# Performance work log

Measured on AMD Instinct MI355X. Metric: run time of the kernel, lower is better.

The kernel has to match this reference:

```python
import jax, jax.numpy as jnp
import numpy as np

B, C, Q, D = 64, 1024, 256, 128
NEG = -1e30  # VERY_NEGATIVE_NUMBER


def setup_inputs() -> dict:
    key = jax.random.key(0)
    k1, k2, k3, k4, k5, k6 = jax.random.split(key, 6)
    return {
        "x_cont": jax.random.normal(k1, (B, C, D), dtype=jnp.float32),
        "x_ques": jax.random.normal(k2, (B, Q, D), dtype=jnp.float32),
        "c_mask": jnp.ones((B, C), dtype=jnp.float32),
        "q_mask": jnp.ones((B, Q), dtype=jnp.float32),
        "W0": jax.random.uniform(k3, (D, 1), jnp.float32, -0.1, 0.1),
        "W1": jax.random.uniform(k4, (D, 1), jnp.float32, -0.1, 0.1),
        "W2": jax.random.uniform(k5, (1, 1, D), jnp.float32, -0.1, 0.1),
        "bias": jnp.zeros((1,), dtype=jnp.float32),
    }


def reference(x_cont, x_ques, c_mask, q_mask, W0, W1, W2, bias):
    # Trilinear similarity S[b,c,q] = x_cont.W0 + x_ques.W1 + (x_cont*W2).x_ques^T + bias
    s0 = x_cont @ W0                                   # [B,C,1]
    s1 = jnp.swapaxes(x_ques @ W1, 1, 2)               # [B,1,Q]
    s2 = jnp.einsum('bcd,bqd->bcq', x_cont * W2, x_ques)  # [B,C,Q]
    S = s0 + s1 + s2 + bias                            # [B,C,Q]

    qm = q_mask[:, None, :]                            # [B,1,Q]
    cm = c_mask[:, :, None]                            # [B,C,1]
    S_ = jax.nn.softmax(S + NEG * (1.0 - qm), axis=-1)           # row softmax [B,C,Q]
    S_T = jnp.swapaxes(jax.nn.softmax(S + NEG * (1.0 - cm), axis=1), 1, 2)  # [B,Q,C]

    c2q = S_ @ x_ques                                  # [B,C,D]
    q2c = (S_ @ S_T) @ x_cont                          # [B,C,D]
    return jnp.concatenate([x_cont, c2q, x_cont * c2q, x_cont * q2c], axis=-1)
```

## Files before the change

### kernel.cpp

```cpp
#include <hip/hip_runtime.h>
#include <math.h>

#define BB 64
#define CC 1024
#define QQ 256
#define DD 128
#define NEGV (-1.0e30f)

typedef short bf8 __attribute__((ext_vector_type(8)));
typedef short bf4 __attribute__((ext_vector_type(4)));
typedef float f4v __attribute__((ext_vector_type(4)));

__device__ __forceinline__ short f2bf(float f) {
    unsigned u = __builtin_bit_cast(unsigned, f);
    u += 0x7FFFu + ((u >> 16) & 1u);
    return (short)(u >> 16);
}
__device__ __forceinline__ float bf2f(short s) {
    unsigned u = ((unsigned)(unsigned short)s) << 16;
    return __builtin_bit_cast(float, u);
}

__global__ __launch_bounds__(256, 2) void k0_all(
        const float* __restrict__ xc, const float* __restrict__ xq,
        const float* __restrict__ W0, const float* __restrict__ W1,
        const float* __restrict__ W2,
        const float* __restrict__ c_mask, const float* __restrict__ q_mask,
        float* __restrict__ s0m, float* __restrict__ s1m,
        short* __restrict__ xc_bf, short* __restrict__ xqw_bf,
        short* __restrict__ xcT_bf, short* __restrict__ xqT_bf) {
    __shared__ float tile[64][129];
    int bid = blockIdx.x;
    const float *src, *W, *mask;
    float* sm; short *rm, *tr;
    int b, tl, R; bool use2;
    if (bid < 1024) {
        b = ((bid >> 7) << 3) | (bid & 7); tl = (bid >> 3) & 15; R = CC;
        src = xc; W = W0; mask = c_mask; sm = s0m; rm = xc_bf; tr = xcT_bf; use2 = false;
    } else {
        int q = bid - 1024;
        b = ((q >> 5) << 3) | (q & 7); tl = (q >> 3) & 3; R = QQ;
        src = xq; W = W1; mask = q_mask; sm = s1m; rm = xqw_bf; tr = xqT_bf; use2 = true;
    }
    int r0 = tl * 64;
    int t = threadIdx.x;
    int c4 = t & 31, rr = t >> 5;
    float4 wv = ((const float4*)W)[c4];
    float4 sc4 = use2 ? ((const float4*)W2)[c4] : make_float4(1.f, 1.f, 1.f, 1.f);
    const float* sb = src + ((size_t)b * R + r0) * DD;
    #pragma unroll
    for (int p = 0; p < 8; ++p) {
        int row = rr + p * 8;
        float4 g = *(const float4*)&sb[(size_t)row * DD + c4 * 4];
        bf4 o;
        o[0] = f2bf(g.x * sc4.x); o[1] = f2bf(g.y * sc4.y);
        o[2] = f2bf(g.z * sc4.z); o[3] = f2bf(g.w * sc4.w);
        *(bf4*)&rm[((size_t)(b * R + r0 + row)) * DD + c4 * 4] = o;
        float part = g.x * wv.x + g.y * wv.y + g.z * wv.z + g.w * wv.w;
        #pragma unroll
        for (int off = 1; off < 32; off <<= 1) part += __shfl_xor(part, off, 64);
        if ((t & 31) == 0)
            sm[(size_t)b * R + r0 + row] =
                part + NEGV * (1.0f - mask[(size_t)b * R + r0 + row]);
        tile[row][c4 * 4 + 0] = g.x; tile[row][c4 * 4 + 1] = g.y;
        tile[row][c4 * 4 + 2] = g.z; tile[row][c4 * 4 + 3] = g.w;
    }
    __syncthreads();
    int rj = (t & 7) * 8;
    #pragma unroll
    for (int pp = 0; pp < 4; ++pp) {
        int d = pp * 32 + (t >> 3);
        bf8 o;
        #pragma unroll
        for (int j = 0; j < 8; ++j) o[j] = f2bf(tile[rj + j][d]);
        *(bf8*)&tr[((size_t)(b * DD + d)) * R + r0 + rj] = o;
    }
}

#define SCP 1032
#define S2P 264

__global__ __launch_bounds__(256, 3) void k1_colsm(
        const short* __restrict__ xc_bf, const short* __restrict__ xcT_bf,
        const short* __restrict__ xqw_bf, const float* __restrict__ s0m,
        short* __restrict__ AT) {
    __shared__ __align__(16) short sc[16][SCP];
    __shared__ float invl[16];

    int bid = blockIdx.x;
    int qt = (bid >> 3) & 15;
    int b = ((bid >> 7) << 3) | (bid & 7);
    int q0 = qt * 16;
    int t = threadIdx.x, w = t >> 6, l = t & 63;
    int quad = l >> 4, l16 = l & 15;

    bf8 bq[4];
    {
        const short* qp = &xqw_bf[(size_t)(b * QQ + q0 + l16) * DD + quad * 8];
        #pragma unroll
        for (int ks = 0; ks < 4; ++ks) bq[ks] = *(const bf8*)&qp[ks * 32];
    }

    const short* abase = &xc_bf[(size_t)(b * CC + w * 16 + l16) * DD + quad * 8];
    const float* s0base = &s0m[b * CC + w * 16 + quad * 4];
    bf8 cur[4];
    #pragma unroll
    for (int ks = 0; ks < 4; ++ks) cur[ks] = *(const bf8*)&abase[ks * 32];
    #pragma unroll
    for (int ct = 0; ct < 16; ++ct) {
        bf8 nxt[4];
        if (ct < 15) {
            const short* ar = abase + (size_t)(ct + 1) * 64 * DD;
            #pragma unroll
            for (int ks = 0; ks < 4; ++ks) nxt[ks] = *(const bf8*)&ar[ks * 32];
        }
        f4v acc = {0.f, 0.f, 0.f, 0.f};
        #pragma unroll
        for (int ks = 0; ks < 4; ++ks)
            acc = __builtin_amdgcn_mfma_f32_16x16x32_bf16(cur[ks], bq[ks], acc, 0, 0, 0);
        f4v s0v = *(const f4v*)&s0base[ct * 64];
        bf4 ov;
        #pragma unroll
        for (int r = 0; r < 4; ++r) ov[r] = f2bf(acc[r] + s0v[r]);
        *(bf4*)&sc[l16][ct * 64 + w * 16 + quad * 4] = ov;
        if (ct < 15) {
            #pragma unroll
            for (int ks = 0; ks < 4; ++ks) cur[ks] = nxt[ks];
        }
    }
    __syncthreads();

    const short* b0base = &xcT_bf[(size_t)(b * DD + w * 32 + l16) * CC + quad * 8];
    const short* b1base = b0base + (size_t)16 * CC;
    bf8 pb[3][4];
    #pragma unroll
    for (int i = 0; i < 3; ++i) {
        #pragma unroll
        for (int ks = 0; ks < 2; ++ks) {
            pb[i][ks]     = *(const bf8*)&b0base[i * 64 + ks * 32];
            pb[i][2 + ks] = *(const bf8*)&b1base[i * 64 + ks * 32];
        }
    }

    {
        int q = t >> 4, k = t & 15;
        float m = -3.0e38f;
        #pragma unroll 8
        for (int i = 0; i < 64; ++i) m = fmaxf(m, bf2f(sc[q][k + 16 * i]));
        #pragma unroll
        for (int off = 1; off < 16; off <<= 1) m = fmaxf(m, __shfl_xor(m, off, 64));
        float sum = 0.f;
        #pragma unroll 8
        for (int i = 0; i < 64; ++i) {
            int idx = k + 16 * i;
            float e = __expf(bf2f(sc[q][idx]) - m);
            sc[q][idx] = f2bf(e);
            sum += e;
        }
        #pragma unroll
        for (int off = 1; off < 16; off <<= 1) sum += __shfl_xor(sum, off, 64);
        if (k == 0) invl[q] = 1.0f / sum;
    }
    __syncthreads();

    f4v acc0 = {0.f, 0.f, 0.f, 0.f}, acc1 = {0.f, 0.f, 0.f, 0.f};
    #pragma unroll
    for (int ct = 0; ct < 16; ++ct) {
        bf8 c00 = pb[0][0], c01 = pb[0][1], c10 = pb[0][2], c11 = pb[0][3];
        #pragma unroll
        for (int i = 0; i < 2; ++i)
            #pragma unroll
            for (int j = 0; j < 4; ++j) pb[i][j] = pb[i + 1][j];
        if (ct + 3 < 16) {
            #pragma unroll
            for (int ks = 0; ks < 2; ++ks) {
                pb[2][ks]     = *(const bf8*)&b0base[(ct + 3) * 64 + ks * 32];
                pb[2][2 + ks] = *(const bf8*)&b1base[(ct + 3) * 64 + ks * 32];
            }
        }
        bf8 a0 = *(const bf8*)&sc[l16][ct * 64 + quad * 8];
        bf8 a1 = *(const bf8*)&sc[l16][ct * 64 + 32 + quad * 8];
        acc0 = __builtin_amdgcn_mfma_f32_16x16x32_bf16(a0, c00, acc0, 0, 0, 0);
        acc0 = __builtin_amdgcn_mfma_f32_16x16x32_bf16(a1, c01, acc0, 0, 0, 0);
        acc1 = __builtin_amdgcn_mfma_f32_16x16x32_bf16(a0, c10, acc1, 0, 0, 0);
        acc1 = __builtin_amdgcn_mfma_f32_16x16x32_bf16(a1, c11, acc1, 0, 0, 0);
    }
    {
        bf4 o0, o1;
        #pragma unroll
        for (int r = 0; r < 4; ++r) {
            float il = invl[quad * 4 + r];
            o0[r] = f2bf(acc0[r] * il);
            o1[r] = f2bf(acc1[r] * il);
        }
        int d0 = w * 32 + l16;
        *(bf4*)&AT[(size_t)(b * DD + d0) * QQ + q0 + quad * 4] = o0;
        *(bf4*)&AT[(size_t)(b * DD + d0 + 16) * QQ + q0 + quad * 4] = o1;
    }
}

__global__ __launch_bounds__(256, 3) void k2_rowsm(
        const float* __restrict__ xc, const short* __restrict__ xc_bf,
        const short* __restrict__ xqw_bf, const short* __restrict__ xqT_bf,
        const short* __restrict__ AT, const float* __restrict__ s1m,
        float* __restrict__ out) {
    __shared__ __align__(16) short sc2[32][S2P];
    __shared__ float invl2[32];

    int bid = blockIdx.x;
    int cb = (bid >> 3) & 31;
    int b = ((bid >> 8) << 3) | (bid & 7);
    int c0g = cb * 32;
    int t = threadIdx.x, w = t >> 6, l = t & 63;
    int quad = l >> 4, l16 = l & 15;

    bf8 bc0[4], bc1[4];
    {
        const short* p0 = &xc_bf[(size_t)(b * CC + c0g + l16) * DD + quad * 8];
        const short* p1 = p0 + 16 * DD;
        #pragma unroll
        for (int ks = 0; ks < 4; ++ks) {
            bc0[ks] = *(const bf8*)&p0[ks * 32];
            bc1[ks] = *(const bf8*)&p1[ks * 32];
        }
    }

    const short* abase = &xqw_bf[(size_t)(b * QQ + w * 16 + l16) * DD + quad * 8];
    const float* s1base = &s1m[b * QQ + w * 16 + quad * 4];
    bf8 cur[4];
    #pragma unroll
    for (int ks = 0; ks < 4; ++ks) cur[ks] = *(const bf8*)&abase[ks * 32];
    #pragma unroll
    for (int qt = 0; qt < 4; ++qt) {
        bf8 nxt[4];
        if (qt < 3) {
            const short* ar = abase + (size_t)(qt + 1) * 64 * DD;
            #pragma unroll
            for (int ks = 0; ks < 4; ++ks) nxt[ks] = *(const bf8*)&ar[ks * 32];
        }
        f4v acc0 = {0.f, 0.f, 0.f, 0.f}, acc1 = {0.f, 0.f, 0.f, 0.f};
        #pragma unroll
        for (int ks = 0; ks < 4; ++ks) {
            acc0 = __builtin_amdgcn_mfma_f32_16x16x32_bf16(cur[ks], bc0[ks], acc0, 0, 0, 0);
            acc1 = __builtin_amdgcn_mfma_f32_16x16x32_bf16(cur[ks], bc1[ks], acc1, 0, 0, 0);
        }
        int qbase = qt * 64 + w * 16 + quad * 4;
        f4v sv = *(const f4v*)&s1base[qt * 64];
        bf4 o0, o1;
        #pragma unroll
        for (int r = 0; r < 4; ++r) {
            o0[r] = f2bf(acc0[r] + sv[r]);
            o1[r] = f2bf(acc1[r] + sv[r]);
        }
        *(bf4*)&sc2[l16][qbase] = o0;
        *(bf4*)&sc2[16 + l16][qbase] = o1;
        if (qt < 3) {
            #pragma unroll
            for (int ks = 0; ks < 4; ++ks) cur[ks] = nxt[ks];
        }
    }
    __syncthreads();

    const short* gq = &xqT_bf[(size_t)(b * DD + w * 32 + l16) * QQ + quad * 8];
    const short* ga = &AT[(size_t)(b * DD + w * 32 + l16) * QQ + quad * 8];
    bf8 pb[3][4];
    #pragma unroll
    for (int i = 0; i < 3; ++i) {
        #pragma unroll
        for (int ks = 0; ks < 2; ++ks) {
            pb[i][ks]     = *(const bf8*)&gq[i * 64 + ks * 32];
            pb[i][2 + ks] = *(const bf8*)&gq[(size_t)16 * QQ + i * 64 + ks * 32];
        }
    }

    {
        int c = t >> 3, k = t & 7;
        float m = -3.0e38f;
        #pragma unroll 8
        for (int i = 0; i < 32; ++i) m = fmaxf(m, bf2f(sc2[c][k + 8 * i]));
        #pragma unroll
        for (int off = 1; off < 8; off <<= 1) m = fmaxf(m, __shfl_xor(m, off, 64));
        float sum = 0.f;
        #pragma unroll 8
        for (int i = 0; i < 32; ++i) {
            int idx = k + 8 * i;
            float e = __expf(bf2f(sc2[c][idx]) - m);
            sc2[c][idx] = f2bf(e);
            sum += e;
        }
        #pragma unroll
        for (int off = 1; off < 8; off <<= 1) sum += __shfl_xor(sum, off, 64);
        if (k == 0) invl2[c] = 1.0f / sum;
    }
    __syncthreads();

    f4v ac[2][2], aq[2][2];
    f4v zz = {0.f, 0.f, 0.f, 0.f};
    #pragma unroll
    for (int i = 0; i < 2; ++i)
        #pragma unroll
        for (int j = 0; j < 2; ++j) { ac[i][j] = zz; aq[i][j] = zz; }
    #pragma unroll
    for (int tl = 0; tl < 8; ++tl) {
        bf8 c00 = pb[0][0], c01 = pb[0][1], c10 = pb[0][2], c11 = pb[0][3];
        #pragma unroll
        for (int i = 0; i < 2; ++i)
            #pragma unroll
            for (int j = 0; j < 4; ++j) pb[i][j] = pb[i + 1][j];
        if (tl + 3 < 8) {
            int nt = tl + 3;
            const short* gs = (nt < 4) ? (gq + (size_t)(nt) * 64)
                                       : (ga + (size_t)(nt - 4) * 64);
            #pragma unroll
            for (int ks = 0; ks < 2; ++ks) {
                pb[2][ks]     = *(const bf8*)&gs[ks * 32];
                pb[2][2 + ks] = *(const bf8*)&gs[(size_t)16 * QQ + ks * 32];
            }
        }
        int qoff = (tl & 3) * 64;
        bf8 a00 = *(const bf8*)&sc2[l16][qoff + quad * 8];
        bf8 a01 = *(const bf8*)&sc2[l16][qoff + 32 + quad * 8];
        bf8 a10 = *(const bf8*)&sc2[16 + l16][qoff + quad * 8];
        bf8 a11 = *(const bf8*)&sc2[16 + l16][qoff + 32 + quad * 8];
        if (tl < 4) {
            ac[0][0] = __builtin_amdgcn_mfma_f32_16x16x32_bf16(a00, c00, ac[0][0], 0, 0, 0);
            ac[0][0] = __builtin_amdgcn_mfma_f32_16x16x32_bf16(a01, c01, ac[0][0], 0, 0, 0);
            ac[0][1] = __builtin_amdgcn_mfma_f32_16x16x32_bf16(a00, c10, ac[0][1], 0, 0, 0);
            ac[0][1] = __builtin_amdgcn_mfma_f32_16x16x32_bf16(a01, c11, ac[0][1], 0, 0, 0);
            ac[1][0] = __builtin_amdgcn_mfma_f32_16x16x32_bf16(a10, c00, ac[1][0], 0, 0, 0);
            ac[1][0] = __builtin_amdgcn_mfma_f32_16x16x32_bf16(a11, c01, ac[1][0], 0, 0, 0);
            ac[1][1] = __builtin_amdgcn_mfma_f32_16x16x32_bf16(a10, c10, ac[1][1], 0, 0, 0);
            ac[1][1] = __builtin_amdgcn_mfma_f32_16x16x32_bf16(a11, c11, ac[1][1], 0, 0, 0);
        } else {
            aq[0][0] = __builtin_amdgcn_mfma_f32_16x16x32_bf16(a00, c00, aq[0][0], 0, 0, 0);
            aq[0][0] = __builtin_amdgcn_mfma_f32_16x16x32_bf16(a01, c01, aq[0][0], 0, 0, 0);
            aq[0][1] = __builtin_amdgcn_mfma_f32_16x16x32_bf16(a00, c10, aq[0][1], 0, 0, 0);
            aq[0][1] = __builtin_amdgcn_mfma_f32_16x16x32_bf16(a01, c11, aq[0][1], 0, 0, 0);
            aq[1][0] = __builtin_amdgcn_mfma_f32_16x16x32_bf16(a10, c00, aq[1][0], 0, 0, 0);
            aq[1][0] = __builtin_amdgcn_mfma_f32_16x16x32_bf16(a11, c01, aq[1][0], 0, 0, 0);
            aq[1][1] = __builtin_amdgcn_mfma_f32_16x16x32_bf16(a10, c10, aq[1][1], 0, 0, 0);
            aq[1][1] = __builtin_amdgcn_mfma_f32_16x16x32_bf16(a11, c11, aq[1][1], 0, 0, 0);
        }
    }

    #pragma unroll
    for (int cf = 0; cf < 2; ++cf)
        #pragma unroll
        for (int r = 0; r < 4; ++r) {
            int cl = cf * 16 + quad * 4 + r;
            int c = c0g + cl;
            float il = invl2[cl];
            const float* xrow = xc + (size_t)(b * CC + c) * DD;
            float* orow = out + (size_t)(b * CC + c) * (4 * DD);
            #pragma unroll
            for (int df = 0; df < 2; ++df) {
                int d = w * 32 + df * 16 + l16;
                float xv = xrow[d];
                float c2v = ac[cf][df][r] * il;
                float q2v = aq[cf][df][r] * il;
                orow[d] = xv;
                orow[DD + d] = c2v;
                orow[2 * DD + d] = xv * c2v;
                orow[3 * DD + d] = xv * q2v;
            }
        }
}

extern "C" void kernel_launch(void* const* d_in, const int* in_sizes, int n_in,
                              void* d_out, int out_size, void* d_ws, size_t ws_size,
                              hipStream_t stream) {
    const float* x_cont = (const float*)d_in[0];
    const float* x_ques = (const float*)d_in[1];
    const float* c_mask = (const float*)d_in[2];
    const float* q_mask = (const float*)d_in[3];
    const float* W0     = (const float*)d_in[4];
    const float* W1     = (const float*)d_in[5];
    const float* W2     = (const float*)d_in[6];
    float* out = (float*)d_out;

    char* ws = (char*)d_ws;
    float* s0m    = (float*)ws;  ws += (size_t)BB * CC * 4;
    float* s1m    = (float*)ws;  ws += (size_t)BB * QQ * 4;
    short* xc_bf  = (short*)ws;  ws += (size_t)BB * CC * DD * 2;
    short* xqw_bf = (short*)ws;  ws += (size_t)BB * QQ * DD * 2;
    short* xcT_bf = (short*)ws;  ws += (size_t)BB * CC * DD * 2;
    short* xqT_bf = (short*)ws;  ws += (size_t)BB * QQ * DD * 2;
    short* AT     = (short*)ws;

    k0_all<<<BB * 16 + BB * 4, 256, 0, stream>>>(x_cont, x_ques, W0, W1, W2,
                                                 c_mask, q_mask, s0m, s1m,
                                                 xc_bf, xqw_bf, xcT_bf, xqT_bf);
    k1_colsm<<<BB * 16, 256, 0, stream>>>(xc_bf, xcT_bf, xqw_bf, s0m, AT);
    k2_rowsm<<<BB * 32, 256, 0, stream>>>(x_cont, xc_bf, xqw_bf, xqT_bf, AT, s1m, out);
}
```

Before: 296.4 us.

## Stage transposed B operands through LDS with coalesced loads in both kernels

Both the column-softmax and row-softmax kernels now load the transposed xc/xq/AT operand tiles with coalesced per-thread 16-byte reads into an LDS staging buffer, then read MFMA fragments from LDS. This replaces the per-lane strided global fragment loads and the register ring buffer. The first GEMM is deepened to four tiles of prefetch, the softmax passes use vectorized bf8 LDS reads and writes, and k2's launch bounds are raised to 4 blocks. The cost is four __syncthreads per pair of tiles and extra LDS usage, which may limit occupancy.

```diff
diff --git a/kernel.cpp b/kernel.cpp
--- a/kernel.cpp
+++ b/kernel.cpp
@@ -79,12 +79,64 @@
 
 #define SCP 1032
 #define S2P 264
+#define XTP 72
+
+#define K1_LDA(G, S, CT)                                                 \
+    {                                                                    \
+        const short* ar_ = abase + (size_t)(CT) * 64 * DD;               \
+        G[0] = *(const bf8*)&ar_[0];  G[1] = *(const bf8*)&ar_[32];      \
+        G[2] = *(const bf8*)&ar_[64]; G[3] = *(const bf8*)&ar_[96];      \
+        S = *(const f4v*)&s0base[(CT) * 64];                             \
+    }
+
+#define K1_STEPA(G, S, CT)                                                            \
+    {                                                                                 \
+        f4v acc = {0.f, 0.f, 0.f, 0.f};                                               \
+        acc = __builtin_amdgcn_mfma_f32_16x16x32_bf16(G[0], bq[0], acc, 0, 0, 0);     \
+        acc = __builtin_amdgcn_mfma_f32_16x16x32_bf16(G[1], bq[1], acc, 0, 0, 0);     \
+        acc = __builtin_amdgcn_mfma_f32_16x16x32_bf16(G[2], bq[2], acc, 0, 0, 0);     \
+        acc = __builtin_amdgcn_mfma_f32_16x16x32_bf16(G[3], bq[3], acc, 0, 0, 0);     \
+        bf4 ov;                                                                       \
+        ov[0] = f2bf(acc[0] + S[0]); ov[1] = f2bf(acc[1] + S[1]);                     \
+        ov[2] = f2bf(acc[2] + S[2]); ov[3] = f2bf(acc[3] + S[3]);                     \
+        *(bf4*)&sc[l16][(CT) * 64 + w * 16 + quad * 4] = ov;                          \
+        if ((CT) + 4 < 16) K1_LDA(G, S, (CT) + 4);                                    \
+    }
+
+#define K1_STG(GS, NXT)                                                  \
+    {                                                                    \
+        *(bf8*)&xct[dr][c8 * 8] = GS[0];                                 \
+        *(bf8*)&xct[dr + 32][c8 * 8] = GS[1];                            \
+        *(bf8*)&xct[dr + 64][c8 * 8] = GS[2];                            \
+        *(bf8*)&xct[dr + 96][c8 * 8] = GS[3];                            \
+        if ((NXT) < 16) {                                                \
+            GS[0] = *(const bf8*)&tbase[(NXT) * 64];                     \
+            GS[1] = *(const bf8*)&tbase[(size_t)32 * CC + (NXT) * 64];   \
+            GS[2] = *(const bf8*)&tbase[(size_t)64 * CC + (NXT) * 64];   \
+            GS[3] = *(const bf8*)&tbase[(size_t)96 * CC + (NXT) * 64];   \
+        }                                                                \
+    }
+
+#define K1_CSTEP(CT)                                                               \
+    {                                                                              \
+        bf8 a0 = *(const bf8*)&sc[l16][(CT) * 64 + quad * 8];                      \
+        bf8 b0 = *(const bf8*)&xct[w * 32 + l16][quad * 8];                        \
+        acc0 = __builtin_amdgcn_mfma_f32_16x16x32_bf16(a0, b0, acc0, 0, 0, 0);     \
+        bf8 b1 = *(const bf8*)&xct[w * 32 + 16 + l16][quad * 8];                   \
+        acc1 = __builtin_amdgcn_mfma_f32_16x16x32_bf16(a0, b1, acc1, 0, 0, 0);     \
+        bf8 a1 = *(const bf8*)&sc[l16][(CT) * 64 + 32 + quad * 8];                 \
+        bf8 b2 = *(const bf8*)&xct[w * 32 + l16][32 + quad * 8];                   \
+        acc0 = __builtin_amdgcn_mfma_f32_16x16x32_bf16(a1, b2, acc0, 0, 0, 0);     \
+        bf8 b3 = *(const bf8*)&xct[w * 32 + 16 + l16][32 + quad * 8];              \
+        acc1 = __builtin_amdgcn_mfma_f32_16x16x32_bf16(a1, b3, acc1, 0, 0, 0);     \
+    }
 
 __global__ __launch_bounds__(256, 3) void k1_colsm(
         const short* __restrict__ xc_bf, const short* __restrict__ xcT_bf,
         const short* __restrict__ xqw_bf, const float* __restrict__ s0m,
         short* __restrict__ AT) {
     __shared__ __align__(16) short sc[16][SCP];
+    __shared__ __align__(16) short xct[DD][XTP];
     __shared__ float invl[16];
 
     int bid = blockIdx.x;
@@ -103,59 +155,54 @@
 
     const short* abase = &xc_bf[(size_t)(b * CC + w * 16 + l16) * DD + quad * 8];
     const float* s0base = &s0m[b * CC + w * 16 + quad * 4];
-    bf8 cur[4];
-    #pragma unroll
-    for (int ks = 0; ks < 4; ++ks) cur[ks] = *(const bf8*)&abase[ks * 32];
-    #pragma unroll
-    for (int ct = 0; ct < 16; ++ct) {
-        bf8 nxt[4];
-        if (ct < 15) {
-            const short* ar = abase + (size_t)(ct + 1) * 64 * DD;
-            #pragma unroll
-            for (int ks = 0; ks < 4; ++ks) nxt[ks] = *(const bf8*)&ar[ks * 32];
-        }
-        f4v acc = {0.f, 0.f, 0.f, 0.f};
-        #pragma unroll
-        for (int ks = 0; ks < 4; ++ks)
-            acc = __builtin_amdgcn_mfma_f32_16x16x32_bf16(cur[ks], bq[ks], acc, 0, 0, 0);
-        f4v s0v = *(const f4v*)&s0base[ct * 64];
-        bf4 ov;
-        #pragma unroll
-        for (int r = 0; r < 4; ++r) ov[r] = f2bf(acc[r] + s0v[r]);
-        *(bf4*)&sc[l16][ct * 64 + w * 16 + quad * 4] = ov;
-        if (ct < 15) {
-            #pragma unroll
-            for (int ks = 0; ks < 4; ++ks) cur[ks] = nxt[ks];
-        }
-    }
+    bf8 gA[4], gB[4], gC[4], gD[4];
+    f4v sA, sB, sC, sD;
+    K1_LDA(gA, sA, 0); K1_LDA(gB, sB, 1); K1_LDA(gC, sC, 2); K1_LDA(gD, sD, 3);
+    #pragma unroll
+    for (int c4t = 0; c4t < 16; c4t += 4) {
+        K1_STEPA(gA, sA, c4t + 0);
+        K1_STEPA(gB, sB, c4t + 1);
+        K1_STEPA(gC, sC, c4t + 2);
+        K1_STEPA(gD, sD, c4t + 3);
+    }
+
+    int c8 = t & 7, dr = t >> 3;
+    const short* tbase = &xcT_bf[(size_t)(b * DD + dr) * CC + c8 * 8];
+    bf8 gS0[4], gS1[4];
+    gS0[0] = *(const bf8*)&tbase[0];
+    gS0[1] = *(const bf8*)&tbase[(size_t)32 * CC];
+    gS0[2] = *(const bf8*)&tbase[(size_t)64 * CC];
+    gS0[3] = *(const bf8*)&tbase[(size_t)96 * CC];
+    gS1[0] = *(const bf8*)&tbase[64];
+    gS1[1] = *(const bf8*)&tbase[(size_t)32 * CC + 64];
+    gS1[2] = *(const bf8*)&tbase[(size_t)64 * CC + 64];
+    gS1[3] = *(const bf8*)&tbase[(size_t)96 * CC + 64];
+
     __syncthreads();
-
-    const short* b0base = &xcT_bf[(size_t)(b * DD + w * 32 + l16) * CC + quad * 8];
-    const short* b1base = b0base + (size_t)16 * CC;
-    bf8 pb[3][4];
-    #pragma unroll
-    for (int i = 0; i < 3; ++i) {
-        #pragma unroll
-        for (int ks = 0; ks < 2; ++ks) {
-            pb[i][ks]     = *(const bf8*)&b0base[i * 64 + ks * 32];
-            pb[i][2 + ks] = *(const bf8*)&b1base[i * 64 + ks * 32];
-        }
-    }
 
     {
         int q = t >> 4, k = t & 15;
+        bf8 v[8];
+        #pragma unroll
+        for (int j = 0; j < 8; ++j) v[j] = *(const bf8*)&sc[q][k * 8 + j * 128];
         float m = -3.0e38f;
-        #pragma unroll 8
-        for (int i = 0; i < 64; ++i) m = fmaxf(m, bf2f(sc[q][k + 16 * i]));
+        #pragma unroll
+        for (int j = 0; j < 8; ++j)
+            #pragma unroll
+            for (int e = 0; e < 8; ++e) m = fmaxf(m, bf2f(v[j][e]));
         #pragma unroll
         for (int off = 1; off < 16; off <<= 1) m = fmaxf(m, __shfl_xor(m, off, 64));
         float sum = 0.f;
-        #pragma unroll 8
-        for (int i = 0; i < 64; ++i) {
-            int idx = k + 16 * i;
-            float e = __expf(bf2f(sc[q][idx]) - m);
-            sc[q][idx] = f2bf(e);
-            sum += e;
+        #pragma unroll
+        for (int j = 0; j < 8; ++j) {
+            bf8 o;
+            #pragma unroll
+            for (int e = 0; e < 8; ++e) {
+                float ex = __expf(bf2f(v[j][e]) - m);
+                sum += ex;
+                o[e] = f2bf(ex);
+            }
+            *(bf8*)&sc[q][k * 8 + j * 128] = o;
         }
         #pragma unroll
         for (int off = 1; off < 16; off <<= 1) sum += __shfl_xor(sum, off, 64);
@@ -165,25 +212,15 @@
 
     f4v acc0 = {0.f, 0.f, 0.f, 0.f}, acc1 = {0.f, 0.f, 0.f, 0.f};
     #pragma unroll
-    for (int ct = 0; ct < 16; ++ct) {
-        bf8 c00 = pb[0][0], c01 = pb[0][1], c10 = pb[0][2], c11 = pb[0][3];
-        #pragma unroll
-        for (int i = 0; i < 2; ++i)
-            #pragma unroll
-            for (int j = 0; j < 4; ++j) pb[i][j] = pb[i + 1][j];
-        if (ct + 3 < 16) {
-            #pragma unroll
-            for (int ks = 0; ks < 2; ++ks) {
-                pb[2][ks]     = *(const bf8*)&b0base[(ct + 3) * 64 + ks * 32];
-                pb[2][2 + ks] = *(const bf8*)&b1base[(ct + 3) * 64 + ks * 32];
-            }
-        }
-        bf8 a0 = *(const bf8*)&sc[l16][ct * 64 + quad * 8];
-        bf8 a1 = *(const bf8*)&sc[l16][ct * 64 + 32 + quad * 8];
-        acc0 = __builtin_amdgcn_mfma_f32_16x16x32_bf16(a0, c00, acc0, 0, 0, 0);
-        acc0 = __builtin_amdgcn_mfma_f32_16x16x32_bf16(a1, c01, acc0, 0, 0, 0);
-        acc1 = __builtin_amdgcn_mfma_f32_16x16x32_bf16(a0, c10, acc1, 0, 0, 0);
-        acc1 = __builtin_amdgcn_mfma_f32_16x16x32_bf16(a1, c11, acc1, 0, 0, 0);
+    for (int ct = 0; ct < 16; ct += 2) {
+        K1_STG(gS0, ct + 2);
+        __syncthreads();
+        K1_CSTEP(ct);
+        __syncthreads();
+        K1_STG(gS1, ct + 3);
+        __syncthreads();
+        K1_CSTEP(ct + 1);
+        __syncthreads();
     }
     {
         bf4 o0, o1;
@@ -199,12 +236,81 @@
     }
 }
 
-__global__ __launch_bounds__(256, 3) void k2_rowsm(
+#define K2_LDA(G, CT)                                                    \
+    {                                                                    \
+        const short* ar_ = abase + (size_t)(CT) * 64 * DD;               \
+        G[0] = *(const bf8*)&ar_[0];  G[1] = *(const bf8*)&ar_[32];      \
+        G[2] = *(const bf8*)&ar_[64]; G[3] = *(const bf8*)&ar_[96];     \
+    }
+
+#define K2_STEP1(G, SV, QT)                                                           \
+    {                                                                                 \
+        f4v acc0 = {0.f, 0.f, 0.f, 0.f}, acc1 = {0.f, 0.f, 0.f, 0.f};                 \
+        acc0 = __builtin_amdgcn_mfma_f32_16x16x32_bf16(G[0], bc0[0], acc0, 0, 0, 0);  \
+        acc1 = __builtin_amdgcn_mfma_f32_16x16x32_bf16(G[0], bc1[0], acc1, 0, 0, 0);  \
+        acc0 = __builtin_amdgcn_mfma_f32_16x16x32_bf16(G[1], bc0[1], acc0, 0, 0, 0);  \
+        acc1 = __builtin_amdgcn_mfma_f32_16x16x32_bf16(G[1], bc1[1], acc1, 0, 0, 0);  \
+        acc0 = __builtin_amdgcn_mfma_f32_16x16x32_bf16(G[2], bc0[2], acc0, 0, 0, 0);  \
+        acc1 = __builtin_amdgcn_mfma_f32_16x16x32_bf16(G[2], bc1[2], acc1, 0, 0, 0);  \
+        acc0 = __builtin_amdgcn_mfma_f32_16x16x32_bf16(G[3], bc0[3], acc0, 0, 0, 0);  \
+        acc1 = __builtin_amdgcn_mfma_f32_16x16x32_bf16(G[3], bc1[3], acc1, 0, 0, 0);  \
+        int qbase_ = (QT) * 64 + w * 16 + quad * 4;                                   \
+        bf4 o0, o1;                                                                   \
+        o0[0] = f2bf(acc0[0] + SV[0]); o0[1] = f2bf(acc0[1] + SV[1]);                 \
+        o0[2] = f2bf(acc0[2] + SV[2]); o0[3] = f2bf(acc0[3] + SV[3]);                 \
+        o1[0] = f2bf(acc1[0] + SV[0]); o1[1] = f2bf(acc1[1] + SV[1]);                 \
+        o1[2] = f2bf(acc1[2] + SV[2]); o1[3] = f2bf(acc1[3] + SV[3]);                 \
+        *(bf4*)&sc2[l16][qbase_] = o0;                                                \
+        *(bf4*)&sc2[16 + l16][qbase_] = o1;                                           \
+    }
+
+#define K2_SRC(NT) ((NT) < 4 ? (qtb + (size_t)(NT) * 64) : (atb + (size_t)((NT) - 4) * 64))
+
+#define K2_STG(GS, NT)                                                   \
+    {                                                                    \
+        *(bf8*)&tT[dr][c8 * 8] = GS[0];                                  \
+        *(bf8*)&tT[dr + 32][c8 * 8] = GS[1];                             \
+        *(bf8*)&tT[dr + 64][c8 * 8] = GS[2];                             \
+        *(bf8*)&tT[dr + 96][c8 * 8] = GS[3];                             \
+        if ((NT) < 8) {                                                  \
+            const short* gs_ = K2_SRC(NT);                               \
+            GS[0] = *(const bf8*)&gs_[0];                                \
+            GS[1] = *(const bf8*)&gs_[(size_t)32 * QQ];                  \
+            GS[2] = *(const bf8*)&gs_[(size_t)64 * QQ];                  \
+            GS[3] = *(const bf8*)&gs_[(size_t)96 * QQ];                  \
+        }                                                                \
+    }
+
+#define K2_CSTEP(TL)                                                                   \
+    {                                                                                  \
+        int qoff_ = ((TL) & 3) * 64;                                                   \
+        _Pragma("unroll")                                                              \
+        for (int ks = 0; ks < 2; ++ks) {                                               \
+            bf8 a0 = *(const bf8*)&sc2[l16][qoff_ + ks * 32 + quad * 8];               \
+            bf8 a1 = *(const bf8*)&sc2[16 + l16][qoff_ + ks * 32 + quad * 8];          \
+            bf8 b0 = *(const bf8*)&tT[w * 32 + l16][ks * 32 + quad * 8];               \
+            bf8 b1 = *(const bf8*)&tT[w * 32 + 16 + l16][ks * 32 + quad * 8];          \
+            if ((TL) < 4) {                                                            \
+                ac[0][0] = __builtin_amdgcn_mfma_f32_16x16x32_bf16(a0, b0, ac[0][0], 0, 0, 0); \
+                ac[0][1] = __builtin_amdgcn_mfma_f32_16x16x32_bf16(a0, b1, ac[0][1], 0, 0, 0); \
+                ac[1][0] = __builtin_amdgcn_mfma_f32_16x16x32_bf16(a1, b0, ac[1][0], 0, 0, 0); \
+                ac[1][1] = __builtin_amdgcn_mfma_f32_16x16x32_bf16(a1, b1, ac[1][1], 0, 0, 0); \
+            } else {                                                                   \
+                aq[0][0] = __builtin_amdgcn_mfma_f32_16x16x32_bf16(a0, b0, aq[0][0], 0, 0, 0); \
+                aq[0][1] = __builtin_amdgcn_mfma_f32_16x16x32_bf16(a0, b1, aq[0][1], 0, 0, 0); \
+                aq[1][0] = __builtin_amdgcn_mfma_f32_16x16x32_bf16(a1, b0, aq[1][0], 0, 0, 0); \
+                aq[1][1] = __builtin_amdgcn_mfma_f32_16x16x32_bf16(a1, b1, aq[1][1], 0, 0, 0); \
+            }                                                                          \
+        }                                                                              \
+    }
+
+__global__ __launch_bounds__(256, 4) void k2_rowsm(
         const float* __restrict__ xc, const short* __restrict__ xc_bf,
         const short* __restrict__ xqw_bf, const short* __restrict__ xqT_bf,
         const short* __restrict__ AT, const float* __restrict__ s1m,
         float* __restrict__ out) {
     __shared__ __align__(16) short sc2[32][S2P];
+    __shared__ __align__(16) short tT[DD][XTP];
     __shared__ float invl2[32];
 
     int bid = blockIdx.x;
@@ -227,66 +333,55 @@
 
     const short* abase = &xqw_bf[(size_t)(b * QQ + w * 16 + l16) * DD + quad * 8];
     const float* s1base = &s1m[b * QQ + w * 16 + quad * 4];
-    bf8 cur[4];
-    #pragma unroll
-    for (int ks = 0; ks < 4; ++ks) cur[ks] = *(const bf8*)&abase[ks * 32];
-    #pragma unroll
-    for (int qt = 0; qt < 4; ++qt) {
-        bf8 nxt[4];
-        if (qt < 3) {
-            const short* ar = abase + (size_t)(qt + 1) * 64 * DD;
-            #pragma unroll
-            for (int ks = 0; ks < 4; ++ks) nxt[ks] = *(const bf8*)&ar[ks * 32];
-        }
-        f4v acc0 = {0.f, 0.f, 0.f, 0.f}, acc1 = {0.f, 0.f, 0.f, 0.f};
-        #pragma unroll
-        for (int ks = 0; ks < 4; ++ks) {
-            acc0 = __builtin_amdgcn_mfma_f32_16x16x32_bf16(cur[ks], bc0[ks], acc0, 0, 0, 0);
-            acc1 = __builtin_amdgcn_mfma_f32_16x16x32_bf16(cur[ks], bc1[ks], acc1, 0, 0, 0);
-        }
-        int qbase = qt * 64 + w * 16 + quad * 4;
-        f4v sv = *(const f4v*)&s1base[qt * 64];
-        bf4 o0, o1;
-        #pragma unroll
-        for (int r = 0; r < 4; ++r) {
-            o0[r] = f2bf(acc0[r] + sv[r]);
-            o1[r] = f2bf(acc1[r] + sv[r]);
-        }
-        *(bf4*)&sc2[l16][qbase] = o0;
-        *(bf4*)&sc2[16 + l16][qbase] = o1;
-        if (qt < 3) {
-            #pragma unroll
-            for (int ks = 0; ks < 4; ++ks) cur[ks] = nxt[ks];
-        }
-    }
+    f4v sv0 = *(const f4v*)&s1base[0];
+    f4v sv1 = *(const f4v*)&s1base[64];
+    f4v sv2 = *(const f4v*)&s1base[128];
+    f4v sv3 = *(const f4v*)&s1base[192];
+    bf8 gA[4], gB[4];
+    K2_LDA(gA, 0); K2_LDA(gB, 1);
+    K2_STEP1(gA, sv0, 0); K2_LDA(gA, 2);
+    K2_STEP1(gB, sv1, 1); K2_LDA(gB, 3);
+    K2_STEP1(gA, sv2, 2);
+    K2_STEP1(gB, sv3, 3);
+
+    int c8 = t & 7, dr = t >> 3;
+    const short* qtb = &xqT_bf[(size_t)(b * DD + dr) * QQ + c8 * 8];
+    const short* atb = &AT[(size_t)(b * DD + dr) * QQ + c8 * 8];
+    bf8 gS0[4], gS1[4];
+    gS0[0] = *(const bf8*)&qtb[0];
+    gS0[1] = *(const bf8*)&qtb[(size_t)32 * QQ];
+    gS0[2] = *(const bf8*)&qtb[(size_t)64 * QQ];
+    gS0[3] = *(const bf8*)&qtb[(size_t)96 * QQ];
+    gS1[0] = *(const bf8*)&qtb[64];
+    gS1[1] = *(const bf8*)&qtb[(size_t)32 * QQ + 64];
+    gS1[2] = *(const bf8*)&qtb[(size_t)64 * QQ + 64];
+    gS1[3] = *(const bf8*)&qtb[(size_t)96 * QQ + 64];
+
     __syncthreads();
-
-    const short* gq = &xqT_bf[(size_t)(b * DD + w * 32 + l16) * QQ + quad * 8];
-    const short* ga = &AT[(size_t)(b * DD + w * 32 + l16) * QQ + quad * 8];
-    bf8 pb[3][4];
-    #pragma unroll
-    for (int i = 0; i < 3; ++i) {
-        #pragma unroll
-        for (int ks = 0; ks < 2; ++ks) {
-            pb[i][ks]     = *(const bf8*)&gq[i * 64 + ks * 32];
-            pb[i][2 + ks] = *(const bf8*)&gq[(size_t)16 * QQ + i * 64 + ks * 32];
-        }
-    }
 
     {
         int c = t >> 3, k = t & 7;
+        bf8 v[4];
+        #pragma unroll
+        for (int j = 0; j < 4; ++j) v[j] = *(const bf8*)&sc2[c][k * 8 + j * 64];
         float m = -3.0e38f;
-        #pragma unroll 8
-        for (int i = 0; i < 32; ++i) m = fmaxf(m, bf2f(sc2[c][k + 8 * i]));
+        #pragma unroll
+        for (int j = 0; j < 4; ++j)
+            #pragma unroll
+            for (int e = 0; e < 8; ++e) m = fmaxf(m, bf2f(v[j][e]));
         #pragma unroll
         for (int off = 1; off < 8; off <<= 1) m = fmaxf(m, __shfl_xor(m, off, 64));
         float sum = 0.f;
-        #pragma unroll 8
-        for (int i = 0; i < 32; ++i) {
-            int idx = k + 8 * i;
-            float e = __expf(bf2f(sc2[c][idx]) - m);
-            sc2[c][idx] = f2bf(e);
-            sum += e;
+        #pragma unroll
+        for (int j = 0; j < 4; ++j) {
+            bf8 o;
+            #pragma unroll
+            for (int e = 0; e < 8; ++e) {
+                float ex = __expf(bf2f(v[j][e]) - m);
+                sum += ex;
+                o[e] = f2bf(ex);
+            }
+            *(bf8*)&sc2[c][k * 8 + j * 64] = o;
         }
         #pragma unroll
         for (int off = 1; off < 8; off <<= 1) sum += __shfl_xor(sum, off, 64);
@@ -301,46 +396,15 @@
         #pragma unroll
         for (int j = 0; j < 2; ++j) { ac[i][j] = zz; aq[i][j] = zz; }
     #pragma unroll
-    for (int tl = 0; tl < 8; ++tl) {
-        bf8 c00 = pb[0][0], c01 = pb[0][1], c10 = pb[0][2], c11 = pb[0][3];
-        #pragma unroll
-        for (int i = 0; i < 2; ++i)
-            #pragma unroll
-            for (int j = 0; j < 4; ++j) pb[i][j] = pb[i + 1][j];
-        if (tl + 3 < 8) {
-            int nt = tl + 3;
-            const short* gs = (nt < 4) ? (gq + (size_t)(nt) * 64)
-                                       : (ga + (size_t)(nt - 4) * 64);
-            #pragma unroll
-            for (int ks = 0; ks < 2; ++ks) {
-                pb[2][ks]     = *(const bf8*)&gs[ks * 32];
-                pb[2][2 + ks] = *(const bf8*)&gs[(size_t)16 * QQ + ks * 32];
-            }
-        }
-        int qoff = (tl & 3) * 64;
-        bf8 a00 = *(const bf8*)&sc2[l16][qoff + quad * 8];
-        bf8 a01 = *(const bf8*)&sc2[l16][qoff + 32 + quad * 8];
-        bf8 a10 = *(const bf8*)&sc2[16 + l16][qoff + quad * 8];
-        bf8 a11 = *(const bf8*)&sc2[16 + l16][qoff + 32 + quad * 8];
-        if (tl < 4) {
-            ac[0][0] = __builtin_amdgcn_mfma_f32_16x16x32_bf16(a00, c00, ac[0][0], 0, 0, 0);
-            ac[0][0] = __builtin_amdgcn_mfma_f32_16x16x32_bf16(a01, c01, ac[0][0], 0, 0, 0);
-            ac[0][1] = __builtin_amdgcn_mfma_f32_16x16x32_bf16(a00, c10, ac[0][1], 0, 0, 0);
-            ac[0][1] = __builtin_amdgcn_mfma_f32_16x16x32_bf16(a01, c11, ac[0][1], 0, 0, 0);
-            ac[1][0] = __builtin_amdgcn_mfma_f32_16x16x32_bf16(a10, c00, ac[1][0], 0, 0, 0);
-            ac[1][0] = __builtin_amdgcn_mfma_f32_16x16x32_bf16(a11, c01, ac[1][0], 0, 0, 0);
-            ac[1][1] = __builtin_amdgcn_mfma_f32_16x16x32_bf16(a10, c10, ac[1][1], 0, 0, 0);
-            ac[1][1] = __builtin_amdgcn_mfma_f32_16x16x32_bf16(a11, c11, ac[1][1], 0, 0, 0);
-        } else {
-            aq[0][0] = __builtin_amdgcn_mfma_f32_16x16x32_bf16(a00, c00, aq[0][0], 0, 0, 0);
-            aq[0][0] = __builtin_amdgcn_mfma_f32_16x16x32_bf16(a01, c01, aq[0][0], 0, 0, 0);
-            aq[0][1] = __builtin_amdgcn_mfma_f32_16x16x32_bf16(a00, c10, aq[0][1], 0, 0, 0);
-            aq[0][1] = __builtin_amdgcn_mfma_f32_16x16x32_bf16(a01, c11, aq[0][1], 0, 0, 0);
-            aq[1][0] = __builtin_amdgcn_mfma_f32_16x16x32_bf16(a10, c00, aq[1][0], 0, 0, 0);
-            aq[1][0] = __builtin_amdgcn_mfma_f32_16x16x32_bf16(a11, c01, aq[1][0], 0, 0, 0);
-            aq[1][1] = __builtin_amdgcn_mfma_f32_16x16x32_bf16(a10, c10, aq[1][1], 0, 0, 0);
-            aq[1][1] = __builtin_amdgcn_mfma_f32_16x16x32_bf16(a11, c11, aq[1][1], 0, 0, 0);
-        }
+    for (int tl = 0; tl < 8; tl += 2) {
+        K2_STG(gS0, tl + 2);
+        __syncthreads();
+        K2_CSTEP(tl);
+        __syncthreads();
+        K2_STG(gS1, tl + 3);
+        __syncthreads();
+        K2_CSTEP(tl + 1);
+        __syncthreads();
     }
 
     #pragma unroll
```

After: 261.2 us. -11.9%, faster.
